# Optimization experiments

Hardware: AMD Instinct MI355X
Metric: run time of the kernel (lower is better)

The kernel has to match this reference:

```python
import jax, jax.numpy as jnp
import numpy as np
from jax import lax

D_MODEL = 1024
D_INNER = 2 * D_MODEL          # expand=2
D_STATE = 16
D_CONV = 4
DT_RANK = 64                   # ceil(1024/16)
DT_MIN = 0.001
DT_MAX = 0.1
BATCH = 4
SEQ = 2048


def setup_inputs() -> dict:
    key = jax.random.key(0)
    ks = jax.random.split(key, 8)
    s = lambda fan_in: 1.0 / np.sqrt(fan_in)
    x = jax.random.normal(ks[0], (BATCH, SEQ, D_MODEL), dtype=jnp.float32)
    # Linear weights stored as (in, out) so y = x @ W
    W_in = jax.random.uniform(ks[1], (D_MODEL, 2 * D_INNER), jnp.float32, -s(D_MODEL), s(D_MODEL))
    conv_w = jax.random.uniform(ks[2], (D_INNER, 1, D_CONV), jnp.float32, -s(D_CONV), s(D_CONV))
    conv_b = jax.random.uniform(ks[3], (D_INNER,), jnp.float32, -s(D_CONV), s(D_CONV))
    W_x = jax.random.uniform(ks[4], (D_INNER, DT_RANK + 2 * D_STATE), jnp.float32, -s(D_INNER), s(D_INNER))
    W_dt = jax.random.uniform(ks[5], (DT_RANK, D_INNER), jnp.float32, -s(DT_RANK), s(DT_RANK))
    b_dt = jax.random.uniform(ks[6], (D_INNER,), jnp.float32, -s(DT_RANK), s(DT_RANK))
    # A = arange(1..d_state) repeated over d_inner; store log(A)
    A_log = jnp.log(jnp.broadcast_to(jnp.arange(1, D_STATE + 1, dtype=jnp.float32), (D_INNER, D_STATE)))
    D_param = jnp.ones((D_INNER,), dtype=jnp.float32)
    W_out = jax.random.uniform(ks[7], (D_INNER, D_MODEL), jnp.float32, -s(D_INNER), s(D_INNER))
    return {"x": x, "W_in": W_in, "conv_w": conv_w, "conv_b": conv_b,
            "W_x": W_x, "W_dt": W_dt, "b_dt": b_dt, "A_log": A_log,
            "D_param": D_param, "W_out": W_out}


def reference(x, W_in, conv_w, conv_b, W_x, W_dt, b_dt, A_log, D_param, W_out):
    # in_proj + split
    xz = x @ W_in                                   # (B, S, 2*d_inner)
    x_branch, z_branch = jnp.split(xz, 2, axis=-1)  # each (B, S, d_inner)

    # causal depthwise conv1d (torch pads d_conv-1 both sides then slices [:seq])
    xc = jnp.pad(x_branch.transpose(0, 2, 1), ((0, 0), (0, 0), (D_CONV - 1, 0)))
    xc = lax.conv_general_dilated(xc, conv_w, (1,), 'VALID',
                                  dimension_numbers=('NCH', 'OIH', 'NCH'),
                                  feature_group_count=D_INNER)
    xc = xc + conv_b[None, :, None]
    x_conv = jax.nn.silu(xc.transpose(0, 2, 1))     # (B, S, d_inner)

    # input-dependent dt, B, C
    x_dbl = x_conv @ W_x                            # (B, S, dt_rank + 2*d_state)
    dt_low = x_dbl[..., :DT_RANK]
    Bm = x_dbl[..., DT_RANK:DT_RANK + D_STATE]      # (B, S, d_state)
    Cm = x_dbl[..., DT_RANK + D_STATE:]             # (B, S, d_state)
    dt = jax.nn.sigmoid(dt_low @ W_dt + b_dt) * (DT_MAX - DT_MIN) + DT_MIN
    dt = jnp.maximum(dt, 1e-4)                      # (B, S, d_inner)

    A = -jnp.exp(A_log)                             # (d_inner, d_state)

    # selective scan over time (n_substeps = 1)
    def step(h, inp):
        dt_t, B_t, C_t, x_t = inp                   # (B,di), (B,ds), (B,ds), (B,di)
        dA = jnp.exp(dt_t[:, :, None] * A[None])    # (B, di, ds)
        h = dA * h + (dt_t * x_t)[:, :, None] * B_t[:, None, :]
        y_t = jnp.sum(h * C_t[:, None, :], axis=-1) # (B, di)
        return h, y_t

    h0 = jnp.zeros((x.shape[0], D_INNER, D_STATE), dtype=x.dtype)
    _, ys = lax.scan(step, h0,
                     (dt.swapaxes(0, 1), Bm.swapaxes(0, 1),
                      Cm.swapaxes(0, 1), x_conv.swapaxes(0, 1)))
    y = ys.swapaxes(0, 1)                           # (B, S, d_inner)

    y = y + x_conv * D_param
    y = y * jax.nn.silu(z_branch)
    return y @ W_out                                # (B, S, d_model)
```

## Files before the change

### kernel.cpp

```cpp
#include <hip/hip_runtime.h>

typedef unsigned short u16;
typedef unsigned int u32;
typedef __attribute__((ext_vector_type(8))) short short8;
typedef __attribute__((ext_vector_type(4))) short short4v;
typedef __attribute__((ext_vector_type(4))) float f32x4;

#define NBATCH 4
#define NSEQ   2048
#define DMODEL 1024
#define DINNER 2048
#define DSTATE 16
#define DTRANK 64
#define ROWS   (NBATCH*NSEQ)
#define NCH    64
#define CLEN   32

__device__ __forceinline__ float b2f(u16 u){ union{u32 i; float f;} v; v.i=((u32)u)<<16; return v.f; }
__device__ __forceinline__ u16 f2b(float f){ union{float f; u32 i;} v; v.f=f; u32 i=v.i; return (u16)((i + 0x7FFFu + ((i>>16)&1u))>>16); }
__device__ __forceinline__ float sigmoidf_(float x){ return 1.0f/(1.0f+__expf(-x)); }

__global__ __launch_bounds__(256) void prep(const u16* __restrict__ x,
    const u16* __restrict__ Win, const u16* __restrict__ convw,
    const u16* __restrict__ Wx, const u16* __restrict__ Wdt,
    const u16* __restrict__ Alog, const u16* __restrict__ Wout,
    const u16* __restrict__ v0, const u16* __restrict__ v1, const u16* __restrict__ v2,
    int* __restrict__ meta){
  __shared__ int vote;
  __shared__ int mxbits;
  const int tid = threadIdx.x;
  const u16* V[3] = {v0, v1, v2};

  const u16* ptrs[6] = {x, Win, convw, Wx, Wdt, Wout};
  const float bounds[6] = {8.f, 0.045f, 0.6f, 0.035f, 0.15f, 0.035f};
  const int slots[6] = {0, 1, 2, 4, 5, 9};
  for (int q = 0; q < 6; q++){
    if (tid == 0) vote = 1;
    __syncthreads();
    int bad = 0;
    for (int i = tid; i < 2048; i += 256){
      float v = fabsf(b2f(ptrs[q][i]));
      if (!(v <= bounds[q])) bad = 1;
    }
    if (bad) atomicAnd(&vote, 0);
    __syncthreads();
    if (tid == 0) meta[slots[q]] = vote;
    __syncthreads();
  }
  if (tid == 0){ u16 u = Alog[1]; meta[7] = (u == 0x3F31 || u == 0x3F32) ? 1 : 0; }

  int iD = -1, fD = 1;
  for (int k = 0; k < 3; k++){
    if (V[k][0] == 0x3F80 && V[k][1] == 0x3F80){ iD = k; fD = 1; }
    else if (V[k][0] == 0 && V[k][1] == 0x3F80 && V[k][2] == 0){ iD = k; fD = 0; }
  }
  if (iD < 0){ iD = 2; fD = 1; }
  int oo[2], no = 0;
  for (int k = 0; k < 3; k++) if (k != iD) oo[no++] = k;
  int fo[2]; float mo[2];
  for (int q = 0; q < 2; q++){
    if (tid == 0) vote = 1;
    __syncthreads();
    int bad = 0;
    for (int i = tid; i < 2048; i += 256){
      float v = fabsf(b2f(V[oo[q]][i]));
      if (!(v <= 0.6f)) bad = 1;
    }
    if (bad) atomicAnd(&vote, 0);
    __syncthreads();
    fo[q] = vote;
    if (tid == 0) mxbits = 0;
    __syncthreads();
    float m = 0.f;
    for (int i = tid; i < 2048; i += 256){
      float v = fabsf(fo[q] ? b2f(V[oo[q]][i]) : ((const float*)V[oo[q]])[i]);
      m = fmaxf(m, v);
    }
    atomicMax(&mxbits, __float_as_int(m));
    __syncthreads();
    mo[q] = __int_as_float(mxbits);
    __syncthreads();
  }
  if (tid == 0){
    int a = (mo[0] > 0.25f) ? 0 : 1;
    meta[10] = oo[a];     meta[3] = fo[a];
    meta[11] = oo[1-a];   meta[6] = fo[1-a];
    meta[12] = iD;        meta[8] = fD;
  }
}

__global__ __launch_bounds__(256) void cvt_bf16(const void* __restrict__ in,
                                                u16* __restrict__ out, long n,
                                                const int* __restrict__ meta, int slot){
  long i = (long)blockIdx.x*256 + threadIdx.x;
  if (i >= n) return;
  if (meta[slot]) out[i] = ((const u16*)in)[i];
  else            out[i] = f2b(((const float*)in)[i]);
}

__global__ __launch_bounds__(256) void cvt_x8(const void* __restrict__ in,
                                              u16* __restrict__ out,
                                              const int* __restrict__ meta){
  long i8 = ((long)blockIdx.x*256 + threadIdx.x)*8;
  if (meta[0]){
    *(short8*)(out + i8) = *(const short8*)((const u16*)in + i8);
  } else {
    const float* f = (const float*)in + i8;
    f32x4 a = *(const f32x4*)f;
    f32x4 b = *(const f32x4*)(f+4);
    short8 o;
    #pragma unroll
    for (int j=0;j<4;j++){ ((u16*)&o)[j] = f2b(a[j]); ((u16*)&o)[4+j] = f2b(b[j]); }
    *(short8*)(out + i8) = o;
  }
}

__global__ __launch_bounds__(256) void cvt_trio(const void* __restrict__ v0,
                                                const void* __restrict__ v1,
                                                const void* __restrict__ v2,
                                                const int* __restrict__ meta,
                                                u16* __restrict__ cbc,
                                                u16* __restrict__ bdtc,
                                                u16* __restrict__ dpc){
  int i = blockIdx.x*256 + threadIdx.x;
  int which = i >> 11, d = i & 2047;
  const void* V[3] = {v0, v1, v2};
  int src, fl; u16* dst;
  if (which == 0){ src = meta[10]; fl = meta[3]; dst = cbc; }
  else if (which == 1){ src = meta[11]; fl = meta[6]; dst = bdtc; }
  else { src = meta[12]; fl = meta[8]; dst = dpc; }
  dst[d] = fl ? ((const u16*)V[src])[d] : f2b(((const float*)V[src])[d]);
}

__global__ __launch_bounds__(256) void transpose_pad(const void* __restrict__ inv,
                                                     u16* __restrict__ out,
                                                     int K, int N, int Nout,
                                                     const int* __restrict__ meta, int slot){
  __shared__ u16 t[32][33];
  const int f = meta[slot];
  const u16*   ib = (const u16*)inv;
  const float* iff = (const float*)inv;
  int k0 = blockIdx.x*32, n0 = blockIdx.y*32;
  int tx = threadIdx.x & 31, ty = threadIdx.x >> 5;
  #pragma unroll
  for (int i=0;i<32;i+=8){
    int k = k0+ty+i, n = n0+tx;
    u16 v = 0;
    if (k<K && n<N) v = f ? ib[(long)k*N+n] : f2b(iff[(long)k*N+n]);
    t[ty+i][tx] = v;
  }
  __syncthreads();
  #pragma unroll
  for (int i=0;i<32;i+=8){
    int n = n0+ty+i, k = k0+tx;
    if (n<Nout && k<K) out[(long)n*K+k] = t[tx][ty+i];
  }
}

template<int MODE>
__global__ __launch_bounds__(256) void gemm_bt(
    const u16* __restrict__ A, int lda,
    const u16* __restrict__ Bt, int K,
    u16* __restrict__ C0, u16* __restrict__ C1, int ldc,
    const u16* __restrict__ bias, float* __restrict__ Cf)
{
  __shared__ u16 sa[128*64];
  __shared__ u16 sb[128*64];
  const int tid = threadIdx.x;
  const int lane = tid & 63;
  const int wave = tid >> 6;
  const int wm = (wave >> 1) * 64;
  const int wn = (wave & 1) * 64;
  const int lane15 = lane & 15;
  const int quad = lane >> 4;
  const long rowBase = (long)blockIdx.y * 128;
  const long colBase = (long)blockIdx.x * 128;

  int kbeg = 0, kend = K;
  if (MODE == 4){
    const int span = K >> 2;
    kbeg = blockIdx.z * span;
    kend = kbeg + span;
    Cf += (long)blockIdx.z * (8192L*128);
  }

  f32x4 acc[4][4];
  #pragma unroll
  for (int i=0;i<4;i++)
    #pragma unroll
    for (int j=0;j<4;j++)
      #pragma unroll
      for (int r=0;r<4;r++) acc[i][j][r]=0.0f;

  const int e  = tid*8;
  const int r0 = e >> 6;
  const int c0 = e & 63;

  for (int kb=kbeg; kb<kend; kb+=64) {
    #pragma unroll
    for (int i=0;i<4;i++){
      const u16* ga = A + (rowBase + r0 + i*32)*lda + kb + c0;
      __builtin_amdgcn_global_load_lds((const __attribute__((address_space(1))) void*)ga,
                                       (__attribute__((address_space(3))) void*)&sa[e + i*2048],
                                       16, 0, 0);
    }
    #pragma unroll
    for (int i=0;i<4;i++){
      const u16* gb = Bt + (colBase + r0 + i*32)*(long)K + kb + c0;
      __builtin_amdgcn_global_load_lds((const __attribute__((address_space(1))) void*)gb,
                                       (__attribute__((address_space(3))) void*)&sb[e + i*2048],
                                       16, 0, 0);
    }
    __syncthreads();
    #pragma unroll
    for (int ko=0; ko<2; ko++){
      const int kk = ko*32 + quad*8;
      short8 af[4], bfr[4];
      #pragma unroll
      for (int i=0;i<4;i++) af[i]  = *(const short8*)&sa[(wm + i*16 + lane15)*64 + kk];
      #pragma unroll
      for (int j=0;j<4;j++) bfr[j] = *(const short8*)&sb[(wn + j*16 + lane15)*64 + kk];
      #pragma unroll
      for (int i=0;i<4;i++)
        #pragma unroll
        for (int j=0;j<4;j++)
          acc[i][j] = __builtin_amdgcn_mfma_f32_16x16x32_bf16(af[i], bfr[j], acc[i][j], 0, 0, 0);
    }
    __syncthreads();
  }

  #pragma unroll
  for (int i=0;i<4;i++){
    #pragma unroll
    for (int j=0;j<4;j++){
      long row = rowBase + wm + i*16 + quad*4;
      long col = colBase + wn + j*16 + lane15;
      #pragma unroll
      for (int r=0;r<4;r++){
        float v = acc[i][j][r];
        long rr = row + r;
        if (MODE == 0) {
          C0[rr*ldc + col] = f2b(v);
        } else if (MODE == 2) {
          float t  = sigmoidf_(v + b2f(bias[col]));
          float dv = fmaxf(t*0.099f + 0.001f, 1e-4f);
          C0[rr*ldc + col] = f2b(dv);
        } else if (MODE == 3 || MODE == 4) {
          Cf[rr*ldc + col] = v;
        }
      }
    }
  }
}

__global__ __launch_bounds__(256) void reduce_xdbl(const float* __restrict__ P,
                                                   u16* __restrict__ out){
  const long i4 = ((long)blockIdx.x*256 + threadIdx.x)*4;
  f32x4 a = *(const f32x4*)(P + i4);
  f32x4 b = *(const f32x4*)(P + 1048576 + i4);
  f32x4 c = *(const f32x4*)(P + 2097152 + i4);
  f32x4 d = *(const f32x4*)(P + 3145728 + i4);
  short4v o;
  #pragma unroll
  for (int j=0;j<4;j++) ((u16*)&o)[j] = f2b(a[j]+b[j]+c[j]+d[j]);
  *(short4v*)(out + i4) = o;
}

template<int MODE>
__global__ __launch_bounds__(512, 2) void gemm256(
    const u16* __restrict__ A, int lda,
    const u16* __restrict__ Bt, int K,
    u16* __restrict__ C0, u16* __restrict__ C1, int ldc,
    float* __restrict__ Cf)
{
  __shared__ u16 sa[2*16384];
  __shared__ u16 sb[2*16384];
  const int tid  = threadIdx.x;
  const int lane = tid & 63;
  const int wm   = (tid >> 6) >> 2;
  const int wn   = (tid >> 6) & 3;
  const int lane15 = lane & 15;
  const int quad   = lane >> 4;

  const int nwg  = gridDim.x * gridDim.y;
  const int orig = blockIdx.y * gridDim.x + blockIdx.x;
  const int swz  = (orig & 7) * (nwg >> 3) + (orig >> 3);
  const int bx   = swz % gridDim.x;
  const int by   = swz / gridDim.x;
  const long rowBase = (long)by * 256;
  const long colBase = (long)bx * 256;

  const int xorv = (lane15 & 7) << 3;
  const int k0   = (quad*8) ^ xorv;
  const int k1   = (32 + quad*8) ^ xorv;
  const int aBase = (wm*128 + lane15) * 64;
  const int bBase = (wn*64  + lane15) * 64;

  const int scol = ((tid & 7) ^ ((tid >> 3) & 7)) << 3;
  const int arow = tid >> 3;
  const int bsub = ((tid >> 8) & 1)*64 + ((tid & 255) >> 3);
  const int bdst = (tid & 7) * 8;

  f32x4 acc[8][4];
  #pragma unroll
  for (int i=0;i<8;i++)
    #pragma unroll
    for (int j=0;j<4;j++)
      #pragma unroll
      for (int r=0;r<4;r++) acc[i][j][r]=0.0f;

  const int nt = K >> 6;

  auto stageA = [&](int buf, int rs, int kb){
    const u16* g = A + (rowBase + rs + arow)*(long)lda + kb + scol;
    __builtin_amdgcn_global_load_lds((const __attribute__((address_space(1))) void*)g,
        (__attribute__((address_space(3))) void*)&sa[buf*16384 + rs*64 + tid*8], 16, 0, 0);
  };
  auto stageB = [&](int buf, int cq, int part, int kb){
    const int row = part*128 + cq*32 + bsub;
    const u16* g = Bt + (colBase + row)*(long)K + kb + scol;
    __builtin_amdgcn_global_load_lds((const __attribute__((address_space(1))) void*)g,
        (__attribute__((address_space(3))) void*)&sb[buf*16384 + row*64 + bdst], 16, 0, 0);
  };

  stageA(0,   0, 0); stageA(0, 128, 0);
  stageB(0, 0, 0, 0); stageB(0, 0, 1, 0);
  stageA(0,  64, 0); stageA(0, 192, 0);
  stageB(0, 1, 0, 0); stageB(0, 1, 1, 0);
  asm volatile("s_waitcnt vmcnt(4)\n\ts_barrier" ::: "memory");

  for (int t = 0; t < nt; ++t){
    const int cur = t & 1, nb = cur ^ 1;
    const int kb2 = (t+1) << 6;
    const bool pf = (t+1 < nt);
    const u16* sA = &sa[cur*16384];
    const u16* sB = &sb[cur*16384];
    short8 a0[4][2], a1[4][2], b0[2][2], b1[2][2];

    #pragma unroll
    for (int i=0;i<4;i++){
      a0[i][0] = *(const short8*)&sA[aBase + i*1024 + k0];
      a0[i][1] = *(const short8*)&sA[aBase + i*1024 + k1];
    }
    #pragma unroll
    for (int j=0;j<2;j++){
      b0[j][0] = *(const short8*)&sB[bBase + j*1024 + k0];
      b0[j][1] = *(const short8*)&sB[bBase + j*1024 + k1];
    }
    if (pf){ stageA(nb, 0, kb2); stageA(nb, 128, kb2); }
    __builtin_amdgcn_s_setprio(1);
    #pragma unroll
    for (int s=0;s<2;s++)
      #pragma unroll
      for (int i=0;i<4;i++)
        #pragma unroll
        for (int j=0;j<2;j++)
          acc[i][j] = __builtin_amdgcn_mfma_f32_16x16x32_bf16(a0[i][s], b0[j][s], acc[i][j], 0, 0, 0);
    __builtin_amdgcn_s_setprio(0);
    asm volatile("s_waitcnt vmcnt(4)\n\ts_barrier" ::: "memory");

    #pragma unroll
    for (int i=0;i<4;i++){
      a1[i][0] = *(const short8*)&sA[aBase + 4096 + i*1024 + k0];
      a1[i][1] = *(const short8*)&sA[aBase + 4096 + i*1024 + k1];
    }
    if (pf){ stageB(nb, 0, 0, kb2); stageB(nb, 0, 1, kb2); }
    __builtin_amdgcn_s_setprio(1);
    #pragma unroll
    for (int s=0;s<2;s++)
      #pragma unroll
      for (int i=0;i<4;i++)
        #pragma unroll
        for (int j=0;j<2;j++)
          acc[4+i][j] = __builtin_amdgcn_mfma_f32_16x16x32_bf16(a1[i][s], b0[j][s], acc[4+i][j], 0, 0, 0);
    __builtin_amdgcn_s_setprio(0);
    asm volatile("s_waitcnt vmcnt(4)\n\ts_barrier" ::: "memory");

    #pragma unroll
    for (int j=0;j<2;j++){
      b1[j][0] = *(const short8*)&sB[bBase + 2048 + j*1024 + k0];
      b1[j][1] = *(const short8*)&sB[bBase + 2048 + j*1024 + k1];
    }
    if (pf){ stageA(nb, 64, kb2); stageA(nb, 192, kb2); }
    __builtin_amdgcn_s_setprio(1);
    #pragma unroll
    for (int s=0;s<2;s++)
      #pragma unroll
      for (int i=0;i<4;i++)
        #pragma unroll
        for (int j=0;j<2;j++)
          acc[i][2+j] = __builtin_amdgcn_mfma_f32_16x16x32_bf16(a0[i][s], b1[j][s], acc[i][2+j], 0, 0, 0);
    __builtin_amdgcn_s_setprio(0);
    asm volatile("s_barrier" ::: "memory");

    if (pf){ stageB(nb, 1, 0, kb2); stageB(nb, 1, 1, kb2); }
    __builtin_amdgcn_s_setprio(1);
    #pragma unroll
    for (int s=0;s<2;s++)
      #pragma unroll
      for (int i=0;i<4;i++)
        #pragma unroll
        for (int j=0;j<2;j++)
          acc[4+i][2+j] = __builtin_amdgcn_mfma_f32_16x16x32_bf16(a1[i][s], b1[j][s], acc[4+i][2+j], 0, 0, 0);
    __builtin_amdgcn_s_setprio(0);
    asm volatile("s_waitcnt vmcnt(4)\n\ts_barrier" ::: "memory");
  }

  #pragma unroll
  for (int i=0;i<8;i++){
    const long row = rowBase + wm*128 + i*16 + quad*4;
    #pragma unroll
    for (int j=0;j<4;j++){
      const long col = colBase + wn*64 + j*16 + lane15;
      #pragma unroll
      for (int r=0;r<4;r++){
        const float v = acc[i][j][r];
        const long rr = row + r;
        if (MODE == 1){
          if (col < 2048) C0[rr*2048 + col] = f2b(v);
          else            C1[rr*2048 + (col-2048)] = f2b(v);
        } else {
          Cf[rr*ldc + col] = v;
        }
      }
    }
  }
}

__global__ __launch_bounds__(256) void conv_silu(const u16* __restrict__ xb,
                                                 const u16* __restrict__ w,
                                                 const u16* __restrict__ bias,
                                                 u16* __restrict__ xc){
  long idx8 = ((long)blockIdx.x*256 + threadIdx.x) * 8;
  int d = (int)(idx8 & (DINNER-1));
  int s = (int)((idx8 >> 11) & (NSEQ-1));
  int b = (int)(idx8 >> 22);

  short8 bv = *(const short8*)(bias + d);
  short8 wv0 = *(const short8*)(w + d*4);
  short8 wv1 = *(const short8*)(w + d*4 + 8);
  short8 wv2 = *(const short8*)(w + d*4 + 16);
  short8 wv3 = *(const short8*)(w + d*4 + 24);
  u16 wl[32];
  #pragma unroll
  for (int q=0;q<8;q++){ wl[q] = ((u16*)&wv0)[q]; wl[8+q] = ((u16*)&wv1)[q];
                         wl[16+q] = ((u16*)&wv2)[q]; wl[24+q] = ((u16*)&wv3)[q]; }

  float acc[8];
  #pragma unroll
  for (int l=0;l<8;l++) acc[l] = b2f(((u16*)&bv)[l]);

  #pragma unroll
  for (int j=0;j<4;j++){
    int t = s - 3 + j;
    if (t >= 0){
      short8 xv = *(const short8*)(xb + ((long)(b*NSEQ + t))*DINNER + d);
      #pragma unroll
      for (int l=0;l<8;l++)
        acc[l] += b2f(((u16*)&xv)[l]) * b2f(wl[l*4 + j]);
    }
  }
  short8 ov;
  #pragma unroll
  for (int l=0;l<8;l++){ float y = acc[l]*sigmoidf_(acc[l]); ((u16*)&ov)[l] = f2b(y); }
  *(short8*)(xc + idx8) = ov;
}

__global__ __launch_bounds__(256) void scan_pass1(const u16* __restrict__ dt,
                                                  const u16* __restrict__ xc,
                                                  const u16* __restrict__ xdbl,
                                                  const u16* __restrict__ Alog,
                                                  float* __restrict__ hend,
                                                  float* __restrict__ sumdt){
  const int tid = threadIdx.x;
  const int d0 = blockIdx.x*1024 + tid*4;
  const int c = blockIdx.y;
  const int b = blockIdx.z;
  __shared__ float sB[CLEN][DSTATE];
  for (int i=tid; i<CLEN*DSTATE; i+=256){
    int t = i >> 4, s = i & 15;
    sB[t][s] = b2f(xdbl[((long)(b*NSEQ + c*CLEN + t))*128 + DTRANK + s]);
  }
  bool fast = true;
  #pragma unroll
  for (int j=0;j<4;j++)
    #pragma unroll
    for (int s=0;s<DSTATE;s++){
      float a = -__expf(b2f(Alog[(d0+j)*DSTATE + s]));
      fast = fast && (fabsf(a + (float)(s+1)) < 0.03f*(float)(s+1));
    }
  __syncthreads();

  float h[4][DSTATE];
  #pragma unroll
  for (int j=0;j<4;j++)
    #pragma unroll
    for (int s=0;s<DSTATE;s++) h[j][s] = 0.0f;
  float sd[4] = {0.f,0.f,0.f,0.f};
  long base = ((long)(b*NSEQ + c*CLEN))*DINNER + d0;
  short4v dt4 = *(const short4v*)(dt + base);
  short4v x4  = *(const short4v*)(xc + base);
  if (fast){
    for (int t=0;t<CLEN;t++){
      long nxt = base + (long)((t+1<CLEN)?(t+1):t)*DINNER;
      short4v dtn = *(const short4v*)(dt + nxt);
      short4v xn  = *(const short4v*)(xc + nxt);
      float B[DSTATE];
      *(f32x4*)&B[0]  = *(const f32x4*)&sB[t][0];
      *(f32x4*)&B[4]  = *(const f32x4*)&sB[t][4];
      *(f32x4*)&B[8]  = *(const f32x4*)&sB[t][8];
      *(f32x4*)&B[12] = *(const f32x4*)&sB[t][12];
      #pragma unroll
      for (int j=0;j<4;j++){
        float dtv = b2f(((u16*)&dt4)[j]);
        float xv  = b2f(((u16*)&x4)[j]);
        float u = dtv*xv;
        sd[j] += dtv;
        float e1 = __expf(-dtv);
        float p = e1;
        #pragma unroll
        for (int s=0;s<DSTATE;s++){
          h[j][s] = fmaf(p, h[j][s], u*B[s]);
          p *= e1;
        }
      }
      dt4 = dtn; x4 = xn;
    }
  } else {
    float Acf[4][DSTATE];
    #pragma unroll
    for (int j=0;j<4;j++)
      #pragma unroll
      for (int s=0;s<DSTATE;s++) Acf[j][s] = -__expf(b2f(Alog[(d0+j)*DSTATE + s]));
    for (int t=0;t<CLEN;t++){
      long nxt = base + (long)((t+1<CLEN)?(t+1):t)*DINNER;
      short4v dtn = *(const short4v*)(dt + nxt);
      short4v xn  = *(const short4v*)(xc + nxt);
      float B[DSTATE];
      *(f32x4*)&B[0]  = *(const f32x4*)&sB[t][0];
      *(f32x4*)&B[4]  = *(const f32x4*)&sB[t][4];
      *(f32x4*)&B[8]  = *(const f32x4*)&sB[t][8];
      *(f32x4*)&B[12] = *(const f32x4*)&sB[t][12];
      #pragma unroll
      for (int j=0;j<4;j++){
        float dtv = b2f(((u16*)&dt4)[j]);
        float xv  = b2f(((u16*)&x4)[j]);
        float u = dtv*xv;
        sd[j] += dtv;
        #pragma unroll
        for (int s=0;s<DSTATE;s++){
          float dA = __expf(dtv * Acf[j][s]);
          h[j][s] = fmaf(dA, h[j][s], u*B[s]);
        }
      }
      dt4 = dtn; x4 = xn;
    }
  }
  #pragma unroll
  for (int j=0;j<4;j++){
    long hidx = ((long)(b*DINNER + d0 + j)*NCH + c)*DSTATE;
    #pragma unroll
    for (int q=0;q<4;q++) *(f32x4*)&hend[hidx + q*4] = *(const f32x4*)&h[j][q*4];
    sumdt[(long)(b*DINNER + d0 + j)*NCH + c] = sd[j];
  }
}

__global__ __launch_bounds__(256) void scan_pass2(float* __restrict__ hend,
                                                  const float* __restrict__ sumdt,
                                                  const u16* __restrict__ Alog){
  long i = (long)blockIdx.x*256 + threadIdx.x;
  int s = (int)(i & 15);
  long bd = i >> 4;
  int d = (int)(bd & (DINNER-1));
  float A = -__expf(b2f(Alog[d*DSTATE + s]));
  float run = 0.0f;
  long base = bd*NCH*DSTATE + s;
  for (int c=0;c<NCH;c++){
    float e = hend[base + (long)c*DSTATE];
    float decay = __expf(A * sumdt[bd*NCH + c]);
    hend[base + (long)c*DSTATE] = run;
    run = run*decay + e;
  }
}

__global__ __launch_bounds__(256) void scan_pass3(const u16* __restrict__ dt,
                                                  u16* __restrict__ xc,
                                                  const u16* __restrict__ zb,
                                                  const u16* __restrict__ xdbl,
                                                  const u16* __restrict__ Alog,
                                                  const u16* __restrict__ Dp,
                                                  const float* __restrict__ hstart){
  const int tid = threadIdx.x;
  const int d0 = blockIdx.x*1024 + tid*4;
  const int c = blockIdx.y;
  const int b = blockIdx.z;
  __shared__ float sB[CLEN][DSTATE];
  __shared__ float sC[CLEN][DSTATE];
  for (int i=tid; i<CLEN*DSTATE; i+=256){
    int t = i >> 4, s = i & 15;
    long rb = ((long)(b*NSEQ + c*CLEN + t))*128;
    sB[t][s] = b2f(xdbl[rb + DTRANK + s]);
    sC[t][s] = b2f(xdbl[rb + DTRANK + DSTATE + s]);
  }
  bool fast = true;
  #pragma unroll
  for (int j=0;j<4;j++)
    #pragma unroll
    for (int s=0;s<DSTATE;s++){
      float a = -__expf(b2f(Alog[(d0+j)*DSTATE + s]));
      fast = fast && (fabsf(a + (float)(s+1)) < 0.03f*(float)(s+1));
    }
  __syncthreads();

  float h[4][DSTATE];
  #pragma unroll
  for (int j=0;j<4;j++){
    long hidx = ((long)(b*DINNER + d0 + j)*NCH + c)*DSTATE;
    #pragma unroll
    for (int q=0;q<4;q++) *(f32x4*)&h[j][q*4] = *(const f32x4*)&hstart[hidx + q*4];
  }
  short4v dp4 = *(const short4v*)(Dp + d0);
  long base = ((long)(b*NSEQ + c*CLEN))*DINNER + d0;
  short4v dt4 = *(const short4v*)(dt + base);
  short4v x4  = *(const short4v*)(xc + base);
  short4v z4  = *(const short4v*)(zb + base);
  if (fast){
    for (int t=0;t<CLEN;t++){
      long nxt = base + (long)((t+1<CLEN)?(t+1):t)*DINNER;
      short4v dtn = *(const short4v*)(dt + nxt);
      short4v xn  = *(const short4v*)(xc + nxt);
      short4v zn  = *(const short4v*)(zb + nxt);
      float B[DSTATE], C[DSTATE];
      *(f32x4*)&B[0]  = *(const f32x4*)&sB[t][0];
      *(f32x4*)&B[4]  = *(const f32x4*)&sB[t][4];
      *(f32x4*)&B[8]  = *(const f32x4*)&sB[t][8];
      *(f32x4*)&B[12] = *(const f32x4*)&sB[t][12];
      *(f32x4*)&C[0]  = *(const f32x4*)&sC[t][0];
      *(f32x4*)&C[4]  = *(const f32x4*)&sC[t][4];
      *(f32x4*)&C[8]  = *(const f32x4*)&sC[t][8];
      *(f32x4*)&C[12] = *(const f32x4*)&sC[t][12];
      short4v ov;
      #pragma unroll
      for (int j=0;j<4;j++){
        float dtv = b2f(((u16*)&dt4)[j]);
        float xv  = b2f(((u16*)&x4)[j]);
        float zv  = b2f(((u16*)&z4)[j]);
        float u = dtv*xv;
        float e1 = __expf(-dtv);
        float gate = zv*sigmoidf_(zv);
        float p = e1;
        float y = 0.0f;
        #pragma unroll
        for (int s=0;s<DSTATE;s++){
          h[j][s] = fmaf(p, h[j][s], u*B[s]);
          y = fmaf(h[j][s], C[s], y);
          p *= e1;
        }
        y = fmaf(xv, b2f(((u16*)&dp4)[j]), y);
        y *= gate;
        ((u16*)&ov)[j] = f2b(y);
      }
      *(short4v*)(xc + base + (long)t*DINNER) = ov;
      dt4 = dtn; x4 = xn; z4 = zn;
    }
  } else {
    float Acf[4][DSTATE];
    #pragma unroll
    for (int j=0;j<4;j++)
      #pragma unroll
      for (int s=0;s<DSTATE;s++) Acf[j][s] = -__expf(b2f(Alog[(d0+j)*DSTATE + s]));
    for (int t=0;t<CLEN;t++){
      long nxt = base + (long)((t+1<CLEN)?(t+1):t)*DINNER;
      short4v dtn = *(const short4v*)(dt + nxt);
      short4v xn  = *(const short4v*)(xc + nxt);
      short4v zn  = *(const short4v*)(zb + nxt);
      float B[DSTATE], C[DSTATE];
      *(f32x4*)&B[0]  = *(const f32x4*)&sB[t][0];
      *(f32x4*)&B[4]  = *(const f32x4*)&sB[t][4];
      *(f32x4*)&B[8]  = *(const f32x4*)&sB[t][8];
      *(f32x4*)&B[12] = *(const f32x4*)&sB[t][12];
      *(f32x4*)&C[0]  = *(const f32x4*)&sC[t][0];
      *(f32x4*)&C[4]  = *(const f32x4*)&sC[t][4];
      *(f32x4*)&C[8]  = *(const f32x4*)&sC[t][8];
      *(f32x4*)&C[12] = *(const f32x4*)&sC[t][12];
      short4v ov;
      #pragma unroll
      for (int j=0;j<4;j++){
        float dtv = b2f(((u16*)&dt4)[j]);
        float xv  = b2f(((u16*)&x4)[j]);
        float zv  = b2f(((u16*)&z4)[j]);
        float u = dtv*xv;
        float gate = zv*sigmoidf_(zv);
        float y = 0.0f;
        #pragma unroll
        for (int s=0;s<DSTATE;s++){
          float dA = __expf(dtv * Acf[j][s]);
          h[j][s] = fmaf(dA, h[j][s], u*B[s]);
          y = fmaf(h[j][s], C[s], y);
        }
        y = fmaf(xv, b2f(((u16*)&dp4)[j]), y);
        y *= gate;
        ((u16*)&ov)[j] = f2b(y);
      }
      *(short4v*)(xc + base + (long)t*DINNER) = ov;
      dt4 = dtn; x4 = xn; z4 = zn;
    }
  }
}

extern "C" void kernel_launch(void* const* d_in, const int* in_sizes, int n_in,
                              void* d_out, int out_size, void* d_ws, size_t ws_size,
                              hipStream_t stream) {
  const void *x=nullptr,*W_in=nullptr,*conv_w=nullptr,*W_x=nullptr,*W_dt=nullptr,
             *A_log=nullptr,*W_out=nullptr;
  const void* v2048[3] = {nullptr,nullptr,nullptr};
  int n2048 = 0;
  for (int i = 0; i < n_in; i++){
    switch (in_sizes[i]){
      case 8388608: x      = d_in[i]; break;
      case 4194304: W_in   = d_in[i]; break;
      case 8192:    conv_w = d_in[i]; break;
      case 196608:  W_x    = d_in[i]; break;
      case 131072:  W_dt   = d_in[i]; break;
      case 32768:   A_log  = d_in[i]; break;
      case 2097152: W_out  = d_in[i]; break;
      case 2048:    if (n2048 < 3) v2048[n2048++] = d_in[i]; break;
      default: break;
    }
  }

  size_t off = 0;
  char* wsb = (char*)d_ws;
  auto take = [&](size_t n){ void* p = wsb + off; off += (n + 255) & ~(size_t)255; return p; };
  u16* Wt_in  = (u16*)take((size_t)4096*1024*2);
  u16* Wt_x   = (u16*)take((size_t)128*2048*2);
  u16* Wt_dt  = (u16*)take((size_t)2048*64*2);
  u16* Wt_out = (u16*)take((size_t)1024*2048*2);
  u16* xb     = (u16*)take((size_t)ROWS*DINNER*2);
  u16* zb     = (u16*)take((size_t)ROWS*DINNER*2);
  u16* xc     = (u16*)take((size_t)ROWS*DINNER*2);
  u16* xdbl   = (u16*)take((size_t)ROWS*128*2);
  char* shr = (char*)take((size_t)ROWS*NCH*DSTATE*4 + (size_t)ROWS*NCH*4 + 4096);
  u16*   xcvt  = (u16*)shr;
  float* hend  = (float*)shr;
  float* sumdt = (float*)(shr + (size_t)ROWS*NCH*DSTATE*4);
  u16* cwc  = (u16*)take(DINNER*4*2);
  u16* cbc  = (u16*)take(DINNER*2);
  u16* bdtc = (u16*)take(DINNER*2);
  u16* alc  = (u16*)take(DINNER*DSTATE*2);
  u16* dpc  = (u16*)take(DINNER*2);
  int* meta = (int*)take(256);
  float* xdp = (float*)take((size_t)4*8192*128*4);
  u16* dtb = xb;

  prep<<<1, 256, 0, stream>>>((const u16*)x, (const u16*)W_in, (const u16*)conv_w,
                              (const u16*)W_x, (const u16*)W_dt, (const u16*)A_log,
                              (const u16*)W_out,
                              (const u16*)v2048[0], (const u16*)v2048[1], (const u16*)v2048[2],
                              meta);

  cvt_x8<<<(ROWS*DMODEL)/(256*8), 256, 0, stream>>>(x, xcvt, meta);
  cvt_bf16<<<32, 256, 0, stream>>>(conv_w, cwc, DINNER*4, meta, 2);
  cvt_bf16<<<128,256, 0, stream>>>(A_log, alc, DINNER*DSTATE, meta, 7);
  cvt_trio<<<24, 256, 0, stream>>>(v2048[0], v2048[1], v2048[2], meta, cbc, bdtc, dpc);

  transpose_pad<<<dim3(32,128), 256, 0, stream>>>(W_in, Wt_in, 1024, 4096, 4096, meta, 1);
  transpose_pad<<<dim3(64,4),   256, 0, stream>>>(W_x,  Wt_x,  2048, 96,   128,  meta, 4);
  transpose_pad<<<dim3(2,64),   256, 0, stream>>>(W_dt, Wt_dt, 64,   2048, 2048, meta, 5);
  transpose_pad<<<dim3(64,32),  256, 0, stream>>>(W_out,Wt_out,2048, 1024, 1024, meta, 9);

  gemm256<1><<<dim3(16,32), 512, 0, stream>>>(xcvt, 1024, Wt_in, 1024, xb, zb, 2048, nullptr);

  conv_silu<<<(ROWS*DINNER)/(256*8), 256, 0, stream>>>(xb, cwc, cbc, xc);

  gemm_bt<4><<<dim3(1,64,4), 256, 0, stream>>>(xc, 2048, Wt_x, 2048, nullptr, nullptr, 128, nullptr, xdp);
  reduce_xdbl<<<1024, 256, 0, stream>>>(xdp, xdbl);

  gemm_bt<2><<<dim3(16,64), 256, 0, stream>>>(xdbl, 128, Wt_dt, 64, dtb, nullptr, 2048, bdtc, nullptr);

  scan_pass1<<<dim3(2,NCH,NBATCH), 256, 0, stream>>>(dtb, xc, xdbl, alc, hend, sumdt);
  scan_pass2<<<(ROWS*DSTATE)/256, 256, 0, stream>>>(hend, sumdt, alc);
  scan_pass3<<<dim3(2,NCH,NBATCH), 256, 0, stream>>>(dtb, xc, zb, xdbl, alc, dpc, hend);

  gemm_bt<3><<<dim3(8,64), 256, 0, stream>>>(xc, 2048, Wt_out, 2048, nullptr, nullptr, 1024, nullptr, (float*)d_out);
}
```

Before: 470.8 us.

## Deepen gemm256 prefetch pipeline and halve channels per thread in scan kernels

The in_proj GEMM main loop is restructured to unroll two K-tiles per iteration. It prefetches the next tile's A/B chunks one stage further ahead, using explicit barrier, lgkmcnt wait and sched_barrier around each MFMA group, so global-to-LDS loads overlap more compute. Separately, the scan pass1/pass3 kernels process 2 channels per thread instead of 4 and launch twice as many blocks, trading wider per-thread work for more parallelism and lower register pressure. The GEMM loop now assumes an even number of K-tiles, and the extra barriers could add sync overhead.

```diff
diff --git a/kernel.cpp b/kernel.cpp
--- a/kernel.cpp
+++ b/kernel.cpp
@@ -4,6 +4,7 @@
 typedef unsigned int u32;
 typedef __attribute__((ext_vector_type(8))) short short8;
 typedef __attribute__((ext_vector_type(4))) short short4v;
+typedef __attribute__((ext_vector_type(2))) short short2v;
 typedef __attribute__((ext_vector_type(4))) float f32x4;
 
 #define NBATCH 4
@@ -266,6 +267,43 @@
   *(short4v*)(out + i4) = o;
 }
 
+template<int IB, int JB>
+__device__ __forceinline__ void mm16(f32x4 (&acc)[8][4],
+                                     const short8 (&Av)[4][2], const short8 (&Bv)[2][2]){
+  #pragma unroll
+  for (int s=0;s<2;s++)
+    #pragma unroll
+    for (int i=0;i<4;i++)
+      #pragma unroll
+      for (int j=0;j<2;j++)
+        acc[IB+i][JB+j] = __builtin_amdgcn_mfma_f32_16x16x32_bf16(Av[i][s], Bv[j][s], acc[IB+i][JB+j], 0, 0, 0);
+}
+
+__device__ __forceinline__ void lda4(short8 (&dst)[4][2], const u16* s, int base, int k0, int k1){
+  #pragma unroll
+  for (int i=0;i<4;i++){
+    dst[i][0] = *(const short8*)&s[base + i*1024 + k0];
+    dst[i][1] = *(const short8*)&s[base + i*1024 + k1];
+  }
+}
+__device__ __forceinline__ void ldb2(short8 (&dst)[2][2], const u16* s, int base, int k0, int k1){
+  #pragma unroll
+  for (int j=0;j<2;j++){
+    dst[j][0] = *(const short8*)&s[base + j*1024 + k0];
+    dst[j][1] = *(const short8*)&s[base + j*1024 + k1];
+  }
+}
+
+#define GB_SYNC_IN()  do{ asm volatile("s_barrier" ::: "memory"); \
+                          asm volatile("s_waitcnt lgkmcnt(0)" ::: "memory"); \
+                          __builtin_amdgcn_sched_barrier(0); \
+                          __builtin_amdgcn_s_setprio(1); }while(0)
+#define GB_SYNC_OUT() do{ __builtin_amdgcn_s_setprio(0); \
+                          asm volatile("s_barrier" ::: "memory"); }while(0)
+#define GB_SYNC_OUT_VM() do{ __builtin_amdgcn_s_setprio(0); \
+                          asm volatile("s_waitcnt vmcnt(6)" ::: "memory"); \
+                          asm volatile("s_barrier" ::: "memory"); }while(0)
+
 template<int MODE>
 __global__ __launch_bounds__(512, 2) void gemm256(
     const u16* __restrict__ A, int lda,
@@ -322,88 +360,46 @@
     __builtin_amdgcn_global_load_lds((const __attribute__((address_space(1))) void*)g,
         (__attribute__((address_space(3))) void*)&sb[buf*16384 + row*64 + bdst], 16, 0, 0);
   };
-
-  stageA(0,   0, 0); stageA(0, 128, 0);
-  stageB(0, 0, 0, 0); stageB(0, 0, 1, 0);
-  stageA(0,  64, 0); stageA(0, 192, 0);
-  stageB(0, 1, 0, 0); stageB(0, 1, 1, 0);
-  asm volatile("s_waitcnt vmcnt(4)\n\ts_barrier" ::: "memory");
-
-  for (int t = 0; t < nt; ++t){
-    const int cur = t & 1, nb = cur ^ 1;
-    const int kb2 = (t+1) << 6;
-    const bool pf = (t+1 < nt);
-    const u16* sA = &sa[cur*16384];
-    const u16* sB = &sb[cur*16384];
-    short8 a0[4][2], a1[4][2], b0[2][2], b1[2][2];
-
-    #pragma unroll
-    for (int i=0;i<4;i++){
-      a0[i][0] = *(const short8*)&sA[aBase + i*1024 + k0];
-      a0[i][1] = *(const short8*)&sA[aBase + i*1024 + k1];
-    }
-    #pragma unroll
-    for (int j=0;j<2;j++){
-      b0[j][0] = *(const short8*)&sB[bBase + j*1024 + k0];
-      b0[j][1] = *(const short8*)&sB[bBase + j*1024 + k1];
-    }
-    if (pf){ stageA(nb, 0, kb2); stageA(nb, 128, kb2); }
-    __builtin_amdgcn_s_setprio(1);
-    #pragma unroll
-    for (int s=0;s<2;s++)
-      #pragma unroll
-      for (int i=0;i<4;i++)
-        #pragma unroll
-        for (int j=0;j<2;j++)
-          acc[i][j] = __builtin_amdgcn_mfma_f32_16x16x32_bf16(a0[i][s], b0[j][s], acc[i][j], 0, 0, 0);
-    __builtin_amdgcn_s_setprio(0);
-    asm volatile("s_waitcnt vmcnt(4)\n\ts_barrier" ::: "memory");
-
-    #pragma unroll
-    for (int i=0;i<4;i++){
-      a1[i][0] = *(const short8*)&sA[aBase + 4096 + i*1024 + k0];
-      a1[i][1] = *(const short8*)&sA[aBase + 4096 + i*1024 + k1];
-    }
-    if (pf){ stageB(nb, 0, 0, kb2); stageB(nb, 0, 1, kb2); }
-    __builtin_amdgcn_s_setprio(1);
-    #pragma unroll
-    for (int s=0;s<2;s++)
-      #pragma unroll
-      for (int i=0;i<4;i++)
-        #pragma unroll
-        for (int j=0;j<2;j++)
-          acc[4+i][j] = __builtin_amdgcn_mfma_f32_16x16x32_bf16(a1[i][s], b0[j][s], acc[4+i][j], 0, 0, 0);
-    __builtin_amdgcn_s_setprio(0);
-    asm volatile("s_waitcnt vmcnt(4)\n\ts_barrier" ::: "memory");
-
-    #pragma unroll
-    for (int j=0;j<2;j++){
-      b1[j][0] = *(const short8*)&sB[bBase + 2048 + j*1024 + k0];
-      b1[j][1] = *(const short8*)&sB[bBase + 2048 + j*1024 + k1];
-    }
-    if (pf){ stageA(nb, 64, kb2); stageA(nb, 192, kb2); }
-    __builtin_amdgcn_s_setprio(1);
-    #pragma unroll
-    for (int s=0;s<2;s++)
-      #pragma unroll
-      for (int i=0;i<4;i++)
-        #pragma unroll
-        for (int j=0;j<2;j++)
-          acc[i][2+j] = __builtin_amdgcn_mfma_f32_16x16x32_bf16(a0[i][s], b1[j][s], acc[i][2+j], 0, 0, 0);
-    __builtin_amdgcn_s_setprio(0);
-    asm volatile("s_barrier" ::: "memory");
-
-    if (pf){ stageB(nb, 1, 0, kb2); stageB(nb, 1, 1, kb2); }
-    __builtin_amdgcn_s_setprio(1);
-    #pragma unroll
-    for (int s=0;s<2;s++)
-      #pragma unroll
-      for (int i=0;i<4;i++)
-        #pragma unroll
-        for (int j=0;j<2;j++)
-          acc[4+i][2+j] = __builtin_amdgcn_mfma_f32_16x16x32_bf16(a1[i][s], b1[j][s], acc[4+i][2+j], 0, 0, 0);
-    __builtin_amdgcn_s_setprio(0);
-    asm volatile("s_waitcnt vmcnt(4)\n\ts_barrier" ::: "memory");
+  auto stageAh = [&](int buf, int h, int kb){ stageA(buf, h*64, kb); stageA(buf, 128 + h*64, kb); };
+  auto stageBc = [&](int buf, int cq, int kb){ stageB(buf, cq, 0, kb); stageB(buf, cq, 1, kb); };
+
+  stageAh(0,0,0);  stageBc(0,0,0);  stageAh(0,1,0);  stageBc(0,1,0);
+  stageAh(1,0,64); stageBc(1,0,64); stageAh(1,1,64);
+  asm volatile("s_waitcnt vmcnt(6)" ::: "memory");
+  asm volatile("s_barrier" ::: "memory");
+
+  const u16* sA0 = &sa[0];      const u16* sB0 = &sb[0];
+  const u16* sA1 = &sa[16384];  const u16* sB1 = &sb[16384];
+  short8 a0[4][2], a1[4][2], b0[2][2], b1[2][2];
+
+  for (int it = 0; it < (nt >> 1); ++it){
+    const int kb = it << 7;
+
+    lda4(a0, sA0, aBase, k0, k1);
+    ldb2(b0, sB0, bBase, k0, k1);
+    stageBc(1, 1, kb + 64);
+    GB_SYNC_IN();  mm16<0,0>(acc, a0, b0);  GB_SYNC_OUT();
+    lda4(a1, sA0, aBase + 4096, k0, k1);
+    stageAh(0, 0, kb + 128);
+    GB_SYNC_IN();  mm16<4,0>(acc, a1, b0);  GB_SYNC_OUT();
+    ldb2(b1, sB0, bBase + 2048, k0, k1);
+    stageBc(0, 0, kb + 128);
+    GB_SYNC_IN();  mm16<0,2>(acc, a0, b1);  GB_SYNC_OUT();
+    stageAh(0, 1, kb + 128);
+    GB_SYNC_IN();  mm16<4,2>(acc, a1, b1);  GB_SYNC_OUT_VM();
+
+    lda4(a0, sA1, aBase, k0, k1);
+    ldb2(b0, sB1, bBase, k0, k1);
+    stageBc(0, 1, kb + 128);
+    GB_SYNC_IN();  mm16<0,0>(acc, a0, b0);  GB_SYNC_OUT();
+    lda4(a1, sA1, aBase + 4096, k0, k1);
+    stageAh(1, 0, kb + 192);
+    GB_SYNC_IN();  mm16<4,0>(acc, a1, b0);  GB_SYNC_OUT();
+    ldb2(b1, sB1, bBase + 2048, k0, k1);
+    stageBc(1, 0, kb + 192);
+    GB_SYNC_IN();  mm16<0,2>(acc, a0, b1);  GB_SYNC_OUT();
+    stageAh(1, 1, kb + 192);
+    GB_SYNC_IN();  mm16<4,2>(acc, a1, b1);  GB_SYNC_OUT_VM();
   }
 
   #pragma unroll
@@ -473,7 +469,7 @@
                                                   float* __restrict__ hend,
                                                   float* __restrict__ sumdt){
   const int tid = threadIdx.x;
-  const int d0 = blockIdx.x*1024 + tid*4;
+  const int d0 = blockIdx.x*512 + tid*2;
   const int c = blockIdx.y;
   const int b = blockIdx.z;
   __shared__ float sB[CLEN][DSTATE];
@@ -483,7 +479,7 @@
   }
   bool fast = true;
   #pragma unroll
-  for (int j=0;j<4;j++)
+  for (int j=0;j<2;j++)
     #pragma unroll
     for (int s=0;s<DSTATE;s++){
       float a = -__expf(b2f(Alog[(d0+j)*DSTATE + s]));
@@ -491,29 +487,29 @@
     }
   __syncthreads();
 
-  float h[4][DSTATE];
-  #pragma unroll
-  for (int j=0;j<4;j++)
+  float h[2][DSTATE];
+  #pragma unroll
+  for (int j=0;j<2;j++)
     #pragma unroll
     for (int s=0;s<DSTATE;s++) h[j][s] = 0.0f;
-  float sd[4] = {0.f,0.f,0.f,0.f};
+  float sd[2] = {0.f,0.f};
   long base = ((long)(b*NSEQ + c*CLEN))*DINNER + d0;
-  short4v dt4 = *(const short4v*)(dt + base);
-  short4v x4  = *(const short4v*)(xc + base);
+  short2v dt2 = *(const short2v*)(dt + base);
+  short2v x2  = *(const short2v*)(xc + base);
   if (fast){
     for (int t=0;t<CLEN;t++){
       long nxt = base + (long)((t+1<CLEN)?(t+1):t)*DINNER;
-      short4v dtn = *(const short4v*)(dt + nxt);
-      short4v xn  = *(const short4v*)(xc + nxt);
+      short2v dtn = *(const short2v*)(dt + nxt);
+      short2v xn  = *(const short2v*)(xc + nxt);
       float B[DSTATE];
       *(f32x4*)&B[0]  = *(const f32x4*)&sB[t][0];
       *(f32x4*)&B[4]  = *(const f32x4*)&sB[t][4];
       *(f32x4*)&B[8]  = *(const f32x4*)&sB[t][8];
       *(f32x4*)&B[12] = *(const f32x4*)&sB[t][12];
       #pragma unroll
-      for (int j=0;j<4;j++){
-        float dtv = b2f(((u16*)&dt4)[j]);
-        float xv  = b2f(((u16*)&x4)[j]);
+      for (int j=0;j<2;j++){
+        float dtv = b2f(((u16*)&dt2)[j]);
+        float xv  = b2f(((u16*)&x2)[j]);
         float u = dtv*xv;
         sd[j] += dtv;
         float e1 = __expf(-dtv);
@@ -524,27 +520,27 @@
           p *= e1;
         }
       }
-      dt4 = dtn; x4 = xn;
+      dt2 = dtn; x2 = xn;
     }
   } else {
-    float Acf[4][DSTATE];
-    #pragma unroll
-    for (int j=0;j<4;j++)
+    float Acf[2][DSTATE];
+    #pragma unroll
+    for (int j=0;j<2;j++)
       #pragma unroll
       for (int s=0;s<DSTATE;s++) Acf[j][s] = -__expf(b2f(Alog[(d0+j)*DSTATE + s]));
     for (int t=0;t<CLEN;t++){
       long nxt = base + (long)((t+1<CLEN)?(t+1):t)*DINNER;
-      short4v dtn = *(const short4v*)(dt + nxt);
-      short4v xn  = *(const short4v*)(xc + nxt);
+      short2v dtn = *(const short2v*)(dt + nxt);
+      short2v xn  = *(const short2v*)(xc + nxt);
       float B[DSTATE];
       *(f32x4*)&B[0]  = *(const f32x4*)&sB[t][0];
       *(f32x4*)&B[4]  = *(const f32x4*)&sB[t][4];
       *(f32x4*)&B[8]  = *(const f32x4*)&sB[t][8];
       *(f32x4*)&B[12] = *(const f32x4*)&sB[t][12];
       #pragma unroll
-      for (int j=0;j<4;j++){
-        float dtv = b2f(((u16*)&dt4)[j]);
-        float xv  = b2f(((u16*)&x4)[j]);
+      for (int j=0;j<2;j++){
+        float dtv = b2f(((u16*)&dt2)[j]);
+        float xv  = b2f(((u16*)&x2)[j]);
         float u = dtv*xv;
         sd[j] += dtv;
         #pragma unroll
@@ -553,11 +549,11 @@
           h[j][s] = fmaf(dA, h[j][s], u*B[s]);
         }
       }
-      dt4 = dtn; x4 = xn;
-    }
-  }
-  #pragma unroll
-  for (int j=0;j<4;j++){
+      dt2 = dtn; x2 = xn;
+    }
+  }
+  #pragma unroll
+  for (int j=0;j<2;j++){
     long hidx = ((long)(b*DINNER + d0 + j)*NCH + c)*DSTATE;
     #pragma unroll
     for (int q=0;q<4;q++) *(f32x4*)&hend[hidx + q*4] = *(const f32x4*)&h[j][q*4];
@@ -591,7 +587,7 @@
                                                   const u16* __restrict__ Dp,
                                                   const float* __restrict__ hstart){
   const int tid = threadIdx.x;
-  const int d0 = blockIdx.x*1024 + tid*4;
+  const int d0 = blockIdx.x*512 + tid*2;
   const int c = blockIdx.y;
   const int b = blockIdx.z;
   __shared__ float sB[CLEN][DSTATE];
@@ -604,7 +600,7 @@
   }
   bool fast = true;
   #pragma unroll
-  for (int j=0;j<4;j++)
+  for (int j=0;j<2;j++)
     #pragma unroll
     for (int s=0;s<DSTATE;s++){
       float a = -__expf(b2f(Alog[(d0+j)*DSTATE + s]));
@@ -612,24 +608,24 @@
     }
   __syncthreads();
 
-  float h[4][DSTATE];
-  #pragma unroll
-  for (int j=0;j<4;j++){
+  float h[2][DSTATE];
+  #pragma unroll
+  for (int j=0;j<2;j++){
     long hidx = ((long)(b*DINNER + d0 + j)*NCH + c)*DSTATE;
     #pragma unroll
     for (int q=0;q<4;q++) *(f32x4*)&h[j][q*4] = *(const f32x4*)&hstart[hidx + q*4];
   }
-  short4v dp4 = *(const short4v*)(Dp + d0);
+  short2v dp2 = *(const short2v*)(Dp + d0);
   long base = ((long)(b*NSEQ + c*CLEN))*DINNER + d0;
-  short4v dt4 = *(const short4v*)(dt + base);
-  short4v x4  = *(const short4v*)(xc + base);
-  short4v z4  = *(const short4v*)(zb + base);
+  short2v dt2 = *(const short2v*)(dt + base);
+  short2v x2  = *(const short2v*)(xc + base);
+  short2v z2  = *(const short2v*)(zb + base);
   if (fast){
     for (int t=0;t<CLEN;t++){
       long nxt = base + (long)((t+1<CLEN)?(t+1):t)*DINNER;
-      short4v dtn = *(const short4v*)(dt + nxt);
-      short4v xn  = *(const short4v*)(xc + nxt);
-      short4v zn  = *(const short4v*)(zb + nxt);
+      short2v dtn = *(const short2v*)(dt + nxt);
+      short2v xn  = *(const short2v*)(xc + nxt);
+      short2v zn  = *(const short2v*)(zb + nxt);
       float B[DSTATE], C[DSTATE];
       *(f32x4*)&B[0]  = *(const f32x4*)&sB[t][0];
       *(f32x4*)&B[4]  = *(const f32x4*)&sB[t][4];
@@ -639,12 +635,12 @@
       *(f32x4*)&C[4]  = *(const f32x4*)&sC[t][4];
       *(f32x4*)&C[8]  = *(const f32x4*)&sC[t][8];
       *(f32x4*)&C[12] = *(const f32x4*)&sC[t][12];
-      short4v ov;
-      #pragma unroll
-      for (int j=0;j<4;j++){
-        float dtv = b2f(((u16*)&dt4)[j]);
-        float xv  = b2f(((u16*)&x4)[j]);
-        float zv  = b2f(((u16*)&z4)[j]);
+      short2v ov;
+      #pragma unroll
+      for (int j=0;j<2;j++){
+        float dtv = b2f(((u16*)&dt2)[j]);
+        float xv  = b2f(((u16*)&x2)[j]);
+        float zv  = b2f(((u16*)&z2)[j]);
         float u = dtv*xv;
         float e1 = __expf(-dtv);
         float gate = zv*sigmoidf_(zv);
@@ -656,24 +652,24 @@
           y = fmaf(h[j][s], C[s], y);
           p *= e1;
         }
-        y = fmaf(xv, b2f(((u16*)&dp4)[j]), y);
+        y = fmaf(xv, b2f(((u16*)&dp2)[j]), y);
         y *= gate;
         ((u16*)&ov)[j] = f2b(y);
       }
-      *(short4v*)(xc + base + (long)t*DINNER) = ov;
-      dt4 = dtn; x4 = xn; z4 = zn;
+      *(short2v*)(xc + base + (long)t*DINNER) = ov;
+      dt2 = dtn; x2 = xn; z2 = zn;
     }
   } else {
-    float Acf[4][DSTATE];
-    #pragma unroll
-    for (int j=0;j<4;j++)
+    float Acf[2][DSTATE];
+    #pragma unroll
+    for (int j=0;j<2;j++)
       #pragma unroll
       for (int s=0;s<DSTATE;s++) Acf[j][s] = -__expf(b2f(Alog[(d0+j)*DSTATE + s]));
     for (int t=0;t<CLEN;t++){
       long nxt = base + (long)((t+1<CLEN)?(t+1):t)*DINNER;
-      short4v dtn = *(const short4v*)(dt + nxt);
-      short4v xn  = *(const short4v*)(xc + nxt);
-      short4v zn  = *(const short4v*)(zb + nxt);
+      short2v dtn = *(const short2v*)(dt + nxt);
+      short2v xn  = *(const short2v*)(xc + nxt);
+      short2v zn  = *(const short2v*)(zb + nxt);
       float B[DSTATE], C[DSTATE];
       *(f32x4*)&B[0]  = *(const f32x4*)&sB[t][0];
       *(f32x4*)&B[4]  = *(const f32x4*)&sB[t][4];
@@ -683,12 +679,12 @@
       *(f32x4*)&C[4]  = *(const f32x4*)&sC[t][4];
       *(f32x4*)&C[8]  = *(const f32x4*)&sC[t][8];
       *(f32x4*)&C[12] = *(const f32x4*)&sC[t][12];
-      short4v ov;
-      #pragma unroll
-      for (int j=0;j<4;j++){
-        float dtv = b2f(((u16*)&dt4)[j]);
-        float xv  = b2f(((u16*)&x4)[j]);
-        float zv  = b2f(((u16*)&z4)[j]);
+      short2v ov;
+      #pragma unroll
+      for (int j=0;j<2;j++){
+        float dtv = b2f(((u16*)&dt2)[j]);
+        float xv  = b2f(((u16*)&x2)[j]);
+        float zv  = b2f(((u16*)&z2)[j]);
         float u = dtv*xv;
         float gate = zv*sigmoidf_(zv);
         float y = 0.0f;
@@ -698,12 +694,12 @@
           h[j][s] = fmaf(dA, h[j][s], u*B[s]);
           y = fmaf(h[j][s], C[s], y);
         }
-        y = fmaf(xv, b2f(((u16*)&dp4)[j]), y);
+        y = fmaf(xv, b2f(((u16*)&dp2)[j]), y);
         y *= gate;
         ((u16*)&ov)[j] = f2b(y);
       }
-      *(short4v*)(xc + base + (long)t*DINNER) = ov;
-      dt4 = dtn; x4 = xn; z4 = zn;
+      *(short2v*)(xc + base + (long)t*DINNER) = ov;
+      dt2 = dtn; x2 = xn; z2 = zn;
     }
   }
 }
@@ -778,9 +774,9 @@
 
   gemm_bt<2><<<dim3(16,64), 256, 0, stream>>>(xdbl, 128, Wt_dt, 64, dtb, nullptr, 2048, bdtc, nullptr);
 
-  scan_pass1<<<dim3(2,NCH,NBATCH), 256, 0, stream>>>(dtb, xc, xdbl, alc, hend, sumdt);
+  scan_pass1<<<dim3(4,NCH,NBATCH), 256, 0, stream>>>(dtb, xc, xdbl, alc, hend, sumdt);
   scan_pass2<<<(ROWS*DSTATE)/256, 256, 0, stream>>>(hend, sumdt, alc);
-  scan_pass3<<<dim3(2,NCH,NBATCH), 256, 0, stream>>>(dtb, xc, zb, xdbl, alc, dpc, hend);
+  scan_pass3<<<dim3(4,NCH,NBATCH), 256, 0, stream>>>(dtb, xc, zb, xdbl, alc, dpc, hend);
 
   gemm_bt<3><<<dim3(8,64), 256, 0, stream>>>(xc, 2048, Wt_out, 2048, nullptr, nullptr, 1024, nullptr, (float*)d_out);
 }
```

After: 485.5 us. +3.1%, slower.
